# Performance work log

Measured on AMD Instinct MI355X. Metric: run time of the kernel, lower is better.

## Reference

```python
import jax, jax.numpy as jnp
import numpy as np
import itertools
jax.config.update("jax_enable_x64", True)

ND, NQ, B = 4, 3, 256          # ndrives, nqubits, batch_size
D = 2 ** NQ                     # Hilbert-space dim = 8


def _pauli_basis(nq):
    I = np.eye(2, dtype=np.complex128)
    X = np.array([[0, 1], [1, 0]], dtype=np.complex128)
    Y = np.array([[0, -1j], [1j, 0]], dtype=np.complex128)
    Z = np.array([[1, 0], [0, -1]], dtype=np.complex128)
    mats = []
    for combo in itertools.product([I, X, Y, Z], repeat=nq):
        m = np.array([[1.0 + 0j]], dtype=np.complex128)
        for s in combo:
            m = np.kron(m, s)
        mats.append(m)
    return np.stack(mats)  # [4**nq, 2**nq, 2**nq], Hermitian


def setup_inputs() -> dict:
    key = jax.random.key(0)
    k1, k2, k3 = jax.random.split(key, 3)
    paulies = jnp.asarray(_pauli_basis(NQ))          # [64, 8, 8] complex128
    L = paulies.shape[0]
    x = jax.random.normal(k1, (B, ND), dtype=jnp.float64)
    # keras 'normal' initializer ~ stddev 0.05
    kernel = 0.05 * jax.random.normal(k2, (ND, L), dtype=jnp.float64)
    bias = 0.05 * jax.random.normal(k3, (L,), dtype=jnp.float64)
    return {"x": x, "kernel": kernel, "bias": bias, "paulies": paulies}


def _probs(pw_i, paulies):
    # pw_i: [L] real pauli weights for one sample
    H = jnp.tensordot(pw_i.astype(jnp.complex128), paulies, axes=[[0], [0]])  # [D, D]
    e, v = jnp.linalg.eigh(H)                      # Hermitian eigendecomp
    expe = jnp.exp(-1j * e)                        # [D]
    # amp_j = sum_s conj(v)[0,s] * exp(-i e_s) * v[j,s]  (evolution of |0>)
    amp = jnp.einsum('s,js->j', jnp.conj(v[0, :]) * expe, v)  # [D]
    return amp.real ** 2 + amp.imag ** 2           # P, [D] float64


def reference(x, kernel, bias, paulies):
    pw = x @ kernel + bias                         # [B, L]
    f = lambda p: _probs(p, paulies)
    P = jax.vmap(f)(pw)                            # [B, D]
    # per-sample Jacobian dP/d(pauli_weights): [B, D, L]
    g = jax.vmap(jax.jacrev(f))(pw)
    oneoverp = 1.0 / P                             # [B, D]
    # chain rule: pw = x @ kernel + bias  =>  dP/dkernel[i,p,j,k] = x[i,j] * g[i,p,k]
    p_k = jnp.einsum('ij,ipk->ipjk', x, g)         # [B, D, ND, L]
    I_k = jnp.einsum('ipjk,iplm,ip->ijklm', p_k, p_k, oneoverp)  # [B, ND, L, ND, L]
    I_b = jnp.einsum('ipj,ipk,ip->ijk', g, g, oneoverp)          # [B, L, L]
    return (I_k, I_b)
```

## Files before the change

### kernel.cpp

```cpp
#include <hip/hip_runtime.h>
#include <math.h>

typedef float f4_t __attribute__((ext_vector_type(4)));

#define NTERM 20
#define TROW  9
#define TMAT  (TROW * 8)

__device__ const float INVFACT[48] = {
  1.0f, 1.0f, 5.0e-1f, 1.66666666666667e-1f, 4.16666666666667e-2f,
  8.33333333333333e-3f, 1.38888888888889e-3f, 1.98412698412698e-4f,
  2.48015873015873e-5f, 2.75573192239859e-6f, 2.75573192239859e-7f,
  2.50521083854417e-8f, 2.08767569878681e-9f, 1.60590438368216e-10f,
  1.14707455977297e-11f, 7.64716373181982e-13f, 4.77947733238738e-14f,
  2.81145725434552e-15f, 1.56192069685862e-16f, 8.22063524662433e-18f,
  4.11031762331216e-19f, 1.95729410633913e-20f, 8.89679139245057e-22f,
  3.86817017063068e-23f, 1.61173757109612e-24f, 6.44695028438447e-26f,
  2.47959626322480e-27f, 9.18368986379555e-29f, 3.27988923706984e-30f,
  1.13099628864477e-31f, 3.76998762881591e-33f, 1.21612504155352e-34f,
  3.80039075485474e-36f, 1.15163356207720e-37f, 3.38715753552116e-39f,
  0.f, 0.f, 0.f, 0.f, 0.f, 0.f, 0.f, 0.f, 0.f, 0.f, 0.f, 0.f, 0.f
};

__device__ __forceinline__ double rdin(const void* p, int idx, bool isdbl) {
  return isdbl ? ((const double*)p)[idx] : (double)((const float*)p)[idx];
}

__device__ __forceinline__ float bpf(int srcl, float v) {
  return __int_as_float(__builtin_amdgcn_ds_bpermute(srcl, __float_as_int(v)));
}

__device__ __forceinline__ void gmul(float& Cr, float& Ci,
                                     float Ar, float Ai, float Br, float Bi,
                                     int r, int c) {
  float nr = 0.f, ni = 0.f;
  #pragma unroll
  for (int u = 0; u < 8; ++u) {
    int sa = ((r << 3) | u) << 2;
    int sb = ((u << 3) | c) << 2;
    float ar = bpf(sa, Ar), ai = bpf(sa, Ai);
    float br = bpf(sb, Br), bi = bpf(sb, Bi);
    nr += ar*br - ai*bi;
    ni += ar*bi + ai*br;
  }
  Cr = nr; Ci = ni;
}

__device__ __forceinline__ void zmul(float& Cr, float& Ci,
                                     float Br, float Bi,
                                     const float2* Zrow, int c) {
  float nr = 0.f, ni = 0.f;
  #pragma unroll
  for (int u = 0; u < 8; ++u) {
    int sb = ((u << 3) | c) << 2;
    float br = bpf(sb, Br), bi = bpf(sb, Bi);
    nr += Zrow[u].x*br - Zrow[u].y*bi;
    ni += Zrow[u].x*bi + Zrow[u].y*br;
  }
  Cr = nr; Ci = ni;
}

__global__ __launch_bounds__(256) void fi_all(
    const void* __restrict__ xv,
    const void* __restrict__ kv,
    const void* __restrict__ bv,
    float* __restrict__ out, int Bn)
{
  const int i    = blockIdx.x;
  const int t    = threadIdx.x;
  const int wv   = t >> 6;
  const int tl   = t & 63;

  __shared__ float2 Tall[NTERM * TMAT];
  __shared__ float2 Rl[NTERM][8];
  __shared__ float2 Ql[8][8][8];
  __shared__ float  ampre[8], ampim[8], invPs[8];
  __shared__ __align__(16) float gk_km[64][8];
  __shared__ __align__(16) float hk_t[8][68];

  const bool isdbl =
      (__ballot(!(fabsf(((const float*)xv)[tl]) < 1e6f)) != 0ull);

  float pwv = (float)rdin(bv, tl, isdbl);
  #pragma unroll
  for (int j = 0; j < 4; ++j)
    pwv += (float)rdin(xv, i*4 + j, isdbl) * (float)rdin(kv, j*64 + tl, isdbl);

  const int r = tl >> 3, c = tl & 7;
  float Zre, Zim;
  {
    int m = r ^ c;
    float hre = 0.f, him = 0.f;
    #pragma unroll
    for (int u = 0; u < 8; ++u) {
      int k = 0; float pr = 1.f, pim = 0.f;
      #pragma unroll
      for (int q = 0; q < 3; ++q) {
        int bit = 2 - q;
        int f  = (m >> bit) & 1;
        int ch = (u >> bit) & 1;
        int rb = (r >> bit) & 1;
        int d  = f ? (ch ? 2 : 1) : (ch ? 3 : 0);
        k = (k << 2) | d;
        if (d == 2) {
          float nr = rb ? -pim : pim;
          float ni = rb ?  pr  : -pr;
          pr = nr; pim = ni;
        } else if (d == 3 && rb) { pr = -pr; pim = -pim; }
      }
      float w = bpf(k << 2, pwv);
      hre += w * pr; him += w * pim;
    }
    Zre = him; Zim = -hre;
  }

  float2 Zrow[8];
  #pragma unroll
  for (int u = 0; u < 8; ++u) {
    int s = ((r << 3) | u) << 2;
    Zrow[u] = make_float2(bpf(s, Zre), bpf(s, Zim));
  }

  float Z2r, Z2i; zmul(Z2r, Z2i, Zre, Zim, Zrow, c);
  if (wv == 0) {
    Tall[0*TMAT + r*TROW + c] = make_float2((r == c) ? 1.f : 0.f, 0.f);
    Tall[1*TMAT + r*TROW + c] = make_float2(Zre, Zim);
    Tall[2*TMAT + r*TROW + c] = make_float2(Z2r, Z2i);
    float cr_ = Z2r, ci_ = Z2i;
    #pragma unroll
    for (int s = 3; s < 5; ++s) {
      float nr_, ni_; zmul(nr_, ni_, cr_, ci_, Zrow, c);
      cr_ = nr_; ci_ = ni_;
      Tall[s*TMAT + r*TROW + c] = make_float2(cr_, ci_);
    }
  } else {
    float Z4r, Z4i; gmul(Z4r, Z4i, Z2r, Z2i, Z2r, Z2i, r, c);
    float Z5r, Z5i; zmul(Z5r, Z5i, Z4r, Z4i, Zrow, c);
    float Cr_, Ci_;
    if (wv == 1) { Cr_ = Z5r; Ci_ = Z5i; }
    else {
      float Z10r, Z10i; gmul(Z10r, Z10i, Z5r, Z5i, Z5r, Z5i, r, c);
      if (wv == 2) { Cr_ = Z10r; Ci_ = Z10i; }
      else         { gmul(Cr_, Ci_, Z10r, Z10i, Z5r, Z5i, r, c); }
    }
    const int base = wv * 5;
    Tall[base*TMAT + r*TROW + c] = make_float2(Cr_, Ci_);
    #pragma unroll
    for (int s = 1; s < 5; ++s) {
      float nr_, ni_; zmul(nr_, ni_, Cr_, Ci_, Zrow, c);
      Cr_ = nr_; Ci_ = ni_;
      Tall[(base + s)*TMAT + r*TROW + c] = make_float2(Cr_, Ci_);
    }
  }
  __syncthreads();

  if (t < NTERM * 8) {
    const int l = t >> 3, b = t & 7;
    float sr = 0.0f, si = 0.0f;
    #pragma unroll
    for (int j = 0; j < NTERM; ++j) {
      float cf = INVFACT[j + l + 1];
      float2 a = Tall[j*TMAT + b*TROW];
      sr += cf * a.x; si += cf * a.y;
    }
    Rl[l][b] = make_float2(sr, si);
  }
  if (t >= 192 && t < 200) {
    const int b = t - 192;
    float ar = 0.0f, ai = 0.0f;
    #pragma unroll
    for (int j = 0; j < NTERM; ++j) {
      float cf = INVFACT[j];
      float2 a = Tall[j*TMAT + b*TROW];
      ar += cf * a.x; ai += cf * a.y;
    }
    ampre[b] = ar; ampim[b] = ai;
    float P = ar*ar + ai*ai;
    invPs[b] = 1.0f / fmaxf(P, 1e-30f);
  }
  __syncthreads();

  {
    const int p  = t >> 5;
    const int a  = (t >> 2) & 7;
    const int b0 = (t & 3) << 1;
    float q0r = 0.f, q0i = 0.f, q1r = 0.f, q1i = 0.f;
    #pragma unroll
    for (int l = 0; l < NTERM; ++l) {
      float2 T  = Tall[l*TMAT + p*TROW + a];
      f4_t  rp  = *(const f4_t*)&Rl[l][b0];
      q0r += T.x*rp.x - T.y*rp.y;  q0i += T.x*rp.y + T.y*rp.x;
      q1r += T.x*rp.z - T.y*rp.w;  q1i += T.x*rp.w + T.y*rp.z;
    }
    Ql[p][a][b0]   = make_float2(q0r, q0i);
    Ql[p][a][b0+1] = make_float2(q1r, q1i);
  }
  __syncthreads();

  {
    const int k  = t & 63;
    const int pg = t >> 6;
    const int p0 = pg << 1, p1 = p0 + 1;
    const int d0 = (k >> 4) & 3, d1 = (k >> 2) & 3, d2 = k & 3;
    const int m = ((((d0 == 1) | (d0 == 2)) ? 1 : 0) << 2)
                | ((((d1 == 1) | (d1 == 2)) ? 1 : 0) << 1)
                |  (((d2 == 1) | (d2 == 2)) ? 1 : 0);
    float S0r = 0.f, S0i = 0.f, S1r = 0.f, S1i = 0.f;
    #pragma unroll
    for (int a = 0; a < 8; ++a) {
      float pr = 1.0f, pim = 0.0f;
      const int dd[3] = {d0, d1, d2};
      #pragma unroll
      for (int q = 0; q < 3; ++q) {
        int rb = (a >> (2 - q)) & 1;
        int d = dd[q];
        if (d == 2) {
          float nr = rb ? -pim : pim;
          float ni = rb ?  pr  : -pr;
          pr = nr; pim = ni;
        } else if (d == 3 && rb) { pr = -pr; pim = -pim; }
      }
      const int b = a ^ m;
      float2 qa = Ql[p0][a][b];
      float2 qb = Ql[p1][a][b];
      S0r += pr*qa.x - pim*qa.y;  S0i += pr*qa.y + pim*qa.x;
      S1r += pr*qb.x - pim*qb.y;  S1i += pr*qb.y + pim*qb.x;
    }
    float g0 = 2.0f * (ampre[p0]*S0i - ampim[p0]*S0r);
    float g1 = 2.0f * (ampre[p1]*S1i - ampim[p1]*S1r);
    *(float2*)&gk_km[k][p0] = make_float2(g0, g1);
    hk_t[p0][k] = g0 * invPs[p0];
    hk_t[p1][k] = g1 * invPs[p1];
  }

  float sc[4];
  {
    float xl = (float)rdin(xv, i*4 + (tl >> 4), isdbl);
    #pragma unroll
    for (int jj = 0; jj < 4; ++jj)
      sc[jj] = xl * (float)rdin(xv, i*4 + jj, isdbl);
  }
  __syncthreads();

  const int m4 = (tl & 15) << 2;
  f4_t hv[8];
  #pragma unroll
  for (int p = 0; p < 8; ++p) hv[p] = *(const f4_t*)&hk_t[p][m4];

  {
    float* ok = out + (size_t)i * 65536;
    #pragma unroll
    for (int it = 0; it < 16; ++it) {
      const int k = it*4 + wv;
      const f4_t ga = *(const f4_t*)&gk_km[k][0];
      const f4_t gb = *(const f4_t*)&gk_km[k][4];
      f4_t acc = ga.x*hv[0] + ga.y*hv[1] + ga.z*hv[2] + ga.w*hv[3]
               + gb.x*hv[4] + gb.y*hv[5] + gb.z*hv[6] + gb.w*hv[7];
      #pragma unroll
      for (int jj = 0; jj < 4; ++jj) {
        f4_t vv = sc[jj] * acc;
        *(f4_t*)(ok + (size_t)jj*16384 + (size_t)k*256 + (size_t)tl*4) = vv;
      }
    }
  }

  {
    float* ob = out + (size_t)Bn * 65536 + (size_t)i * 4096;
    #pragma unroll
    for (int rr = 0; rr < 4; ++rr) {
      const int k = rr*16 + (t >> 4);
      const f4_t ga = *(const f4_t*)&gk_km[k][0];
      const f4_t gb = *(const f4_t*)&gk_km[k][4];
      f4_t acc = ga.x*hv[0] + ga.y*hv[1] + ga.z*hv[2] + ga.w*hv[3]
               + gb.x*hv[4] + gb.y*hv[5] + gb.z*hv[6] + gb.w*hv[7];
      *(f4_t*)(ob + (size_t)rr*1024 + (size_t)t*4) = acc;
    }
  }
}

extern "C" void kernel_launch(void* const* d_in, const int* in_sizes, int n_in,
                              void* d_out, int out_size, void* d_ws, size_t ws_size,
                              hipStream_t stream) {
  (void)n_in; (void)d_ws; (void)ws_size; (void)out_size;
  int Bn = in_sizes[0] / 4;
  fi_all<<<Bn, 256, 0, stream>>>(d_in[0], d_in[1], d_in[2], (float*)d_out, Bn);
}
```

Baseline: 91.23 us.

## Split big I_k output store into separate wide-grid kernel

Splits the fused kernel in two. The first kernel does the eigen solve and writes only the I_b block (M = g·h). A second kernel with 16x more blocks reads M back from the output buffer, scales it by x_j·x_l, and writes the large I_k tensor. The aim is to spread the dominant 64 MB store over many more blocks than the 256 the batch gives, so bandwidth can be saturated. The cost is an extra launch and a re-read of M from global memory.

Measured after the change: 94.54 us. 1.04x slower.

```diff
diff --git a/kernel.cpp b/kernel.cpp
--- a/kernel.cpp
+++ b/kernel.cpp
@@ -60,7 +60,7 @@
   Cr = nr; Ci = ni;
 }
 
-__global__ __launch_bounds__(256) void fi_all(
+__global__ __launch_bounds__(256) void fi_solve(
     const void* __restrict__ xv,
     const void* __restrict__ kv,
     const void* __restrict__ bv,
@@ -232,38 +232,12 @@
     hk_t[p0][k] = g0 * invPs[p0];
     hk_t[p1][k] = g1 * invPs[p1];
   }
-
-  float sc[4];
-  {
-    float xl = (float)rdin(xv, i*4 + (tl >> 4), isdbl);
-    #pragma unroll
-    for (int jj = 0; jj < 4; ++jj)
-      sc[jj] = xl * (float)rdin(xv, i*4 + jj, isdbl);
-  }
   __syncthreads();
 
   const int m4 = (tl & 15) << 2;
   f4_t hv[8];
   #pragma unroll
   for (int p = 0; p < 8; ++p) hv[p] = *(const f4_t*)&hk_t[p][m4];
-
-  {
-    float* ok = out + (size_t)i * 65536;
-    #pragma unroll
-    for (int it = 0; it < 16; ++it) {
-      const int k = it*4 + wv;
-      const f4_t ga = *(const f4_t*)&gk_km[k][0];
-      const f4_t gb = *(const f4_t*)&gk_km[k][4];
-      f4_t acc = ga.x*hv[0] + ga.y*hv[1] + ga.z*hv[2] + ga.w*hv[3]
-               + gb.x*hv[4] + gb.y*hv[5] + gb.z*hv[6] + gb.w*hv[7];
-      #pragma unroll
-      for (int jj = 0; jj < 4; ++jj) {
-        f4_t vv = sc[jj] * acc;
-        *(f4_t*)(ok + (size_t)jj*16384 + (size_t)k*256 + (size_t)tl*4) = vv;
-      }
-    }
-  }
-
   {
     float* ob = out + (size_t)Bn * 65536 + (size_t)i * 4096;
     #pragma unroll
@@ -278,10 +252,51 @@
   }
 }
 
+__global__ __launch_bounds__(256) void fi_store(
+    const void* __restrict__ xv,
+    float* __restrict__ out, int Bn)
+{
+  const int bx  = blockIdx.x;
+  const int i   = bx >> 4;
+  const int blk = bx & 15;
+  const int t   = threadIdx.x;
+  const int wv  = t >> 6;
+  const int tl  = t & 63;
+
+  __shared__ __align__(16) float Ms[16][68];
+
+  const bool isdbl =
+      (__ballot(!(fabsf(((const float*)xv)[tl]) < 1e6f)) != 0ull);
+
+  const int rg = t >> 4;
+  const int q4 = (t & 15) << 2;
+  const float* Mg = out + (size_t)Bn * 65536 + (size_t)i * 4096;
+  *(f4_t*)&Ms[rg][q4] =
+      *(const f4_t*)(Mg + (size_t)(((blk & 3) << 4) + rg) * 64 + q4);
+
+  const int j = blk >> 2;
+  float sc;
+  {
+    float xj = (float)rdin(xv, i*4 + j, isdbl);
+    sc = xj * (float)rdin(xv, i*4 + (tl >> 4), isdbl);
+  }
+  __syncthreads();
+
+  float* ok = out + (size_t)i * 65536 + (size_t)blk * 4096;
+  #pragma unroll
+  for (int it = 0; it < 4; ++it) {
+    const int kk = it*4 + wv;
+    const f4_t mv = *(const f4_t*)&Ms[kk][q4];
+    f4_t vv = sc * mv;
+    *(f4_t*)(ok + (size_t)kk*256 + (size_t)tl*4) = vv;
+  }
+}
+
 extern "C" void kernel_launch(void* const* d_in, const int* in_sizes, int n_in,
                               void* d_out, int out_size, void* d_ws, size_t ws_size,
                               hipStream_t stream) {
   (void)n_in; (void)d_ws; (void)ws_size; (void)out_size;
   int Bn = in_sizes[0] / 4;
-  fi_all<<<Bn, 256, 0, stream>>>(d_in[0], d_in[1], d_in[2], (float*)d_out, Bn);
-}
+  fi_solve<<<Bn, 256, 0, stream>>>(d_in[0], d_in[1], d_in[2], (float*)d_out, Bn);
+  fi_store<<<Bn * 16, 256, 0, stream>>>(d_in[0], (float*)d_out, Bn);
+}
```
